# Performance work log

Hardware: AMD Instinct MI355X
Metric: run time of the kernel (lower is better)

## Reference

```python
import jax, jax.numpy as jnp
import numpy as np

GRID_SIZE = 5
SPLINE_ORDER = 3
N_COEFF = GRID_SIZE + SPLINE_ORDER  # 8 basis functions per input feature
D_MODEL = 1024
D_FF = 4096


def make_grid(in_features):
    # uniform grid on [-1, 1] extended by spline_order knots each side
    h = 2.0 / GRID_SIZE
    g = np.arange(-SPLINE_ORDER, GRID_SIZE + SPLINE_ORDER + 1, dtype=np.float32) * h - 1.0
    return jnp.asarray(np.tile(g[None, :], (in_features, 1)))  # (in, G + 2k + 1)


def b_splines(x, grid):
    # x: (N, in) -> (N, in, G + k) via Cox-de Boor recursion
    xe = x[..., None]
    bases = ((xe >= grid[:, :-1]) & (xe < grid[:, 1:])).astype(x.dtype)
    for j in range(1, SPLINE_ORDER + 1):
        left = (xe - grid[:, : -(j + 1)]) / (grid[:, j:-1] - grid[:, : -(j + 1)])
        right = (grid[:, j + 1 :] - xe) / (grid[:, j + 1 :] - grid[:, 1:-j])
        bases = left * bases[..., :-1] + right * bases[..., 1:]
    return bases


def kan_linear(x, base_w, spline_w, grid):
    # x: (N, in); base_w: (out, in); spline_w: (out, in, C)
    base = jax.nn.silu(x) @ base_w.T
    b = b_splines(x, grid)                      # (N, in, C)
    spl = jnp.einsum('nic,oic->no', b, spline_w)
    return base + spl


def setup_inputs() -> dict:
    key = jax.random.key(0)
    ks = jax.random.split(key, 7)
    s_in = 1.0 / np.sqrt(D_MODEL)
    s_ff = 1.0 / np.sqrt(D_FF)
    return {
        'x': jax.random.normal(ks[0], (2, 2048, D_MODEL), jnp.float32),
        'base_w1': jax.random.normal(ks[1], (D_FF, D_MODEL), jnp.float32) * s_in,
        'spline_w1': jax.random.normal(ks[2], (D_FF, D_MODEL, N_COEFF), jnp.float32) * s_in * 0.1,
        'base_w2': jax.random.normal(ks[3], (D_FF, D_MODEL), jnp.float32) * s_in,
        'spline_w2': jax.random.normal(ks[4], (D_FF, D_MODEL, N_COEFF), jnp.float32) * s_in * 0.1,
        'base_w3': jax.random.normal(ks[5], (D_MODEL, D_FF), jnp.float32) * s_ff,
        'spline_w3': jax.random.normal(ks[6], (D_MODEL, D_FF, N_COEFF), jnp.float32) * s_ff * 0.1,
        'grid_in': make_grid(D_MODEL),
        'grid_ff': make_grid(D_FF),
    }


def reference(x, base_w1, spline_w1, base_w2, spline_w2, base_w3, spline_w3, grid_in, grid_ff):
    shp = x.shape
    x2 = x.reshape(-1, shp[-1])                      # (N, d_model)
    h = kan_linear(x2, base_w1, spline_w1, grid_in) * kan_linear(x2, base_w2, spline_w2, grid_in)
    out = kan_linear(h, base_w3, spline_w3, grid_ff)
    return out.reshape(shp)
```

## Files before the change

### kernel.cpp

```cpp
#include <hip/hip_runtime.h>
#include <hip/hip_bf16.h>
#include <cstdint>
#include <cstddef>
#include <type_traits>


#define D_MODEL 1024
#define D_FF    4096
#define NTOK    4096
#define NC      9
#define K1      (D_MODEL * NC)
#define K3      (D_FF * NC)
#define SPLITK2 16
#define SPLITKF 4
#define CHUNK   1024
#define SLOT    65536

typedef __attribute__((ext_vector_type(8))) short bf16x8;
typedef __attribute__((ext_vector_type(4))) float f32x4;

__device__ __forceinline__ unsigned short bf16b(float f) {
  __hip_bfloat16 h = __float2bfloat16(f);
  return __builtin_bit_cast(unsigned short, h);
}

__device__ __forceinline__ void kan_feat_u(float x, unsigned short* dst) {
  float s = x / (1.0f + __expf(-x));
  float B[11];
#pragma unroll
  for (int j = 0; j < 11; ++j) {
    float gj = -2.2f + 0.4f * j;
    B[j] = (x >= gj && x < gj + 0.4f) ? 1.0f : 0.0f;
  }
#pragma unroll
  for (int p = 1; p <= 3; ++p) {
    float inv = 1.0f / (0.4f * p);
#pragma unroll
    for (int i = 0; i + p < 11; ++i) {
      float gi = -2.2f + 0.4f * i;
      B[i] = (x - gi) * inv * B[i] + ((gi + 0.4f + 0.4f * p) - x) * inv * B[i + 1];
    }
  }
  dst[0] = bf16b(s);
#pragma unroll
  for (int c = 0; c < 8; ++c) dst[1 + c] = bf16b(B[c]);
}

__global__ void pack_kan_w(const float* __restrict__ bw, const float* __restrict__ sw,
                           __hip_bfloat16* __restrict__ W, int K, int inShift,
                           int rowMul, int rowBase, size_t totalPairs) {
  size_t t = (size_t)blockIdx.x * blockDim.x + threadIdx.x;
  if (t >= totalPairs) return;
  size_t o = t >> (inShift - 1);
  size_t ip = (t & (((size_t)1 << (inShift - 1)) - 1)) * 2;
  size_t e0 = (o << inShift) + ip;
  float2 b = *(const float2*)(bw + e0);
  const float4* sp = (const float4*)(sw + e0 * 8);
  float4 s0 = sp[0], s1 = sp[1], s2 = sp[2], s3 = sp[3];
  unsigned short h[18];
  h[0] = bf16b(b.x);
  h[1] = bf16b(s0.x); h[2] = bf16b(s0.y); h[3] = bf16b(s0.z); h[4] = bf16b(s0.w);
  h[5] = bf16b(s1.x); h[6] = bf16b(s1.y); h[7] = bf16b(s1.z); h[8] = bf16b(s1.w);
  h[9] = bf16b(b.y);
  h[10] = bf16b(s2.x); h[11] = bf16b(s2.y); h[12] = bf16b(s2.z); h[13] = bf16b(s2.w);
  h[14] = bf16b(s3.x); h[15] = bf16b(s3.y); h[16] = bf16b(s3.z); h[17] = bf16b(s3.w);
  uint32_t* dst = (uint32_t*)(W + (o * rowMul + rowBase) * (size_t)K + ip * NC);
#pragma unroll
  for (int k = 0; k < 9; ++k) dst[k] = (uint32_t)h[2 * k] | ((uint32_t)h[2 * k + 1] << 16);
}

__global__ void build_a1(const float* __restrict__ x, __hip_bfloat16* __restrict__ A1) {
  size_t t = (size_t)blockIdx.x * blockDim.x + threadIdx.x;
  if (t >= (size_t)NTOK * D_MODEL / 2) return;
  size_t n = t >> 9;
  size_t ip = (t & 511) * 2;
  float2 xv = *(const float2*)(x + n * D_MODEL + ip);
  unsigned short h[18];
  kan_feat_u(xv.x, h);
  kan_feat_u(xv.y, h + 9);
  uint32_t* dst = (uint32_t*)(A1 + n * (size_t)K1 + ip * NC);
#pragma unroll
  for (int k = 0; k < 9; ++k) dst[k] = (uint32_t)h[2 * k] | ((uint32_t)h[2 * k + 1] << 16);
}

template <typename HT>
__global__ void glu_a3(const HT* __restrict__ Hc, __hip_bfloat16* __restrict__ A3c) {
  size_t t = (size_t)blockIdx.x * blockDim.x + threadIdx.x;
  if (t >= (size_t)CHUNK * D_FF / 2) return;
  size_t n = t >> 11;
  size_t jp = (t & 2047) * 2;
  float a0, a1, c0, c1;
  if constexpr (std::is_same<HT, float>::value) {
    float2 u = *(const float2*)(Hc + n * 8192 + jp);
    float2 v = *(const float2*)(Hc + n * 8192 + 4096 + jp);
    a0 = u.x; a1 = u.y; c0 = v.x; c1 = v.y;
  } else {
    a0 = __bfloat162float(Hc[n * 8192 + jp]);
    a1 = __bfloat162float(Hc[n * 8192 + jp + 1]);
    c0 = __bfloat162float(Hc[n * 8192 + 4096 + jp]);
    c1 = __bfloat162float(Hc[n * 8192 + 4096 + jp + 1]);
  }
  unsigned short h[18];
  kan_feat_u(a0 * c0, h);
  kan_feat_u(a1 * c1, h + 9);
  uint32_t* dst = (uint32_t*)(A3c + n * (size_t)K3 + jp * NC);
#pragma unroll
  for (int k = 0; k < 9; ++k) dst[k] = (uint32_t)h[2 * k] | ((uint32_t)h[2 * k + 1] << 16);
}

#define STAGE(Ts)                                                                        \
  {                                                                                      \
    const int _sl = ((Ts) & 1) * SLOT;                                                   \
    const size_t _ko = (size_t)(Ts) * 128;                                               \
    _Pragma("unroll") for (int _st = 0; _st < 4; ++_st) {                                \
      __builtin_amdgcn_global_load_lds(                                                  \
          (const __attribute__((address_space(1))) void*)(gA0 + _st * strideK + _ko),    \
          (__attribute__((address_space(3))) void*)(lds_raw + _sl + _st * 8192 + dW),    \
          16, 0, 0);                                                                     \
      __builtin_amdgcn_global_load_lds(                                                  \
          (const __attribute__((address_space(1))) void*)(gB0 + _st * strideK + _ko),    \
          (__attribute__((address_space(3))) void*)(lds_raw + _sl + 32768 +              \
                                                    _st * 8192 + dW),                    \
          16, 0, 0);                                                                     \
    }                                                                                    \
  }

template <typename CT, bool FUSE>
__global__ __launch_bounds__(512, 2) void gemm256(
    const __hip_bfloat16* __restrict__ A, const __hip_bfloat16* __restrict__ Bw,
    CT* __restrict__ Cp, int N, int K, int kLen,
    __hip_bfloat16* __restrict__ A3out) {
  __shared__ __align__(16) char lds_raw[2 * SLOT];

  const int tid = threadIdx.x;
  const int wid = tid >> 6, lane = tid & 63;
  const int wr = wid >> 2, wc = wid & 3;

  const int nwg = gridDim.x * gridDim.y;
  const int orig = blockIdx.y * gridDim.x + blockIdx.x;
  const int q = nwg >> 3, r = nwg & 7;
  const int xcd = orig & 7, lid = orig >> 3;
  const int wg = (xcd < r ? xcd * (q + 1) : r * (q + 1) + (xcd - r) * q) + lid;
  const int bx = wg % gridDim.x, by = wg / gridDim.x;

  const size_t brow = (size_t)by * 256;
  const size_t bcol = (size_t)bx * 256;
  const int kStart = (int)blockIdx.z * kLen;
  const int NT = kLen / 64;

  const int kbx = (lane & 7) ^ (lane >> 3);
  const int rsub = lane >> 3;
  const size_t strideK = (size_t)K * 128;
  const char* gA0 = (const char*)A +
      ((brow + (size_t)(wid * 8 + rsub)) * (size_t)K + kStart + kbx * 8) * 2;
  const char* gB0 = (const char*)Bw +
      ((bcol + (size_t)(wid * 8 + rsub)) * (size_t)K + kStart + kbx * 8) * 2;
  const int dW = wid * 1024;

  const int gx0 = (((lane >> 4) ^ (lane & 7))) * 16;
  const int gx1 = ((((lane >> 4) + 4) ^ (lane & 7))) * 16;
  const int arow = (wr * 128 + (lane & 15)) * 128;
  const int brw = 32768 + (wc * 64 + (lane & 15)) * 128;

  f32x4 acc[8][4] = {};

  STAGE(0);
  asm volatile("s_waitcnt vmcnt(0)" ::: "memory");
  __builtin_amdgcn_s_barrier();

  for (int T = 0; T < NT; ++T) {
    if (T + 1 < NT) STAGE(T + 1);

    const int sl = (T & 1) * SLOT;
    bf16x8 af[8], bfr[4];
#pragma unroll
    for (int mf = 0; mf < 8; ++mf)
      af[mf] = *(const bf16x8*)(lds_raw + sl + arow + mf * 2048 + gx0);
#pragma unroll
    for (int nf = 0; nf < 4; ++nf)
      bfr[nf] = *(const bf16x8*)(lds_raw + sl + brw + nf * 2048 + gx0);
    __builtin_amdgcn_s_setprio(1);
#pragma unroll
    for (int mf = 0; mf < 8; ++mf)
#pragma unroll
      for (int nf = 0; nf < 4; ++nf)
        acc[mf][nf] =
            __builtin_amdgcn_mfma_f32_16x16x32_bf16(af[mf], bfr[nf], acc[mf][nf], 0, 0, 0);
    __builtin_amdgcn_s_setprio(0);
#pragma unroll
    for (int mf = 0; mf < 8; ++mf)
      af[mf] = *(const bf16x8*)(lds_raw + sl + arow + mf * 2048 + gx1);
#pragma unroll
    for (int nf = 0; nf < 4; ++nf)
      bfr[nf] = *(const bf16x8*)(lds_raw + sl + brw + nf * 2048 + gx1);
    __builtin_amdgcn_s_setprio(1);
#pragma unroll
    for (int mf = 0; mf < 8; ++mf)
#pragma unroll
      for (int nf = 0; nf < 4; ++nf)
        acc[mf][nf] =
            __builtin_amdgcn_mfma_f32_16x16x32_bf16(af[mf], bfr[nf], acc[mf][nf], 0, 0, 0);
    __builtin_amdgcn_s_setprio(0);

    asm volatile("s_waitcnt vmcnt(0)" ::: "memory");
    asm volatile("s_waitcnt lgkmcnt(0)" ::: "memory");
    __builtin_amdgcn_s_barrier();
  }

  if constexpr (FUSE) {
    float* gbuf = (float*)lds_raw;
#pragma unroll
    for (int mf = 0; mf < 8; ++mf) {
      const int s = wr * 8 + mf;
#pragma unroll
      for (int nf = 0; nf < 4; ++nf) {
#pragma unroll
        for (int rr = 0; rr < 4; ++rr) {
          float v = acc[mf][nf][rr];
          float w = __shfl_xor(v, 1, 64);
          if (!(lane & 1)) {
            const int r4 = (lane >> 4) * 4 + rr;
            const int ploc = wc * 32 + nf * 8 + ((lane & 14) >> 1);
            gbuf[s * 2048 + r4 * 128 + ploc] = v * w;
          }
        }
      }
    }
    __builtin_amdgcn_s_barrier();
    const int p2 = tid & 63;
    const int rb = tid >> 6;
    for (int k = 0; k < 32; ++k) {
      const int rr_ = rb + 8 * k;
      const int s = rr_ >> 4, rl = rr_ & 15;
      float g0 = gbuf[s * 2048 + rl * 128 + 2 * p2];
      float g1 = gbuf[s * 2048 + rl * 128 + 2 * p2 + 1];
      unsigned short h[18];
      kan_feat_u(g0, h);
      kan_feat_u(g1, h + 9);
      const size_t n = brow + rr_;
      const size_t pg = (bcol >> 1) + 2 * p2;
      uint32_t* dst = (uint32_t*)(A3out + n * (size_t)K3 + pg * NC);
#pragma unroll
      for (int qq = 0; qq < 9; ++qq)
        dst[qq] = (uint32_t)h[2 * qq] | ((uint32_t)h[2 * qq + 1] << 16);
    }
  } else {
#pragma unroll
    for (int mf = 0; mf < 8; ++mf)
#pragma unroll
      for (int nf = 0; nf < 4; ++nf) {
        const size_t r0 = brow + wr * 128 + mf * 16 + (lane >> 4) * 4;
        const size_t c0 = bcol + wc * 64 + nf * 16 + (lane & 15);
        const size_t M = (size_t)gridDim.y * 256;
        CT* C = Cp + (size_t)blockIdx.z * M * (size_t)N;
#pragma unroll
        for (int rr = 0; rr < 4; ++rr) {
          float v = acc[mf][nf][rr];
          if constexpr (std::is_same<CT, float>::value)
            C[(r0 + rr) * (size_t)N + c0] = v;
          else
            C[(r0 + rr) * (size_t)N + c0] = __float2bfloat16(v);
        }
      }
  }
}

__global__ void reduceK(const float* __restrict__ P, float* __restrict__ out,
                        size_t quarter, int nslice) {
  size_t t = (size_t)blockIdx.x * blockDim.x + threadIdx.x;
  if (t >= quarter) return;
  const float4* p = (const float4*)P;
  float4 a = p[t];
  for (int s = 1; s < nslice; ++s) {
    float4 b = p[(size_t)s * quarter + t];
    a.x += b.x; a.y += b.y; a.z += b.z; a.w += b.w;
  }
  ((float4*)out)[t] = a;
}

extern "C" void kernel_launch(void* const* d_in, const int* in_sizes, int n_in,
                              void* d_out, int out_size, void* d_ws, size_t ws_size,
                              hipStream_t stream) {
  const float* x   = (const float*)d_in[0];
  const float* bw1 = (const float*)d_in[1];
  const float* sw1 = (const float*)d_in[2];
  const float* bw2 = (const float*)d_in[3];
  const float* sw2 = (const float*)d_in[4];
  const float* bw3 = (const float*)d_in[5];
  const float* sw3 = (const float*)d_in[6];
  float* out = (float*)d_out;
  char* ws = (char*)d_ws;

  const size_t W12_B  = (size_t)8192 * K1 * 2;
  const size_t A1_B   = (size_t)NTOK * K1 * 2;
  const size_t A3F_B  = (size_t)NTOK * K3 * 2;
  const size_t A3C_B  = (size_t)CHUNK * K3 * 2;
  const size_t HF32_B = (size_t)NTOK * 8192 * 4;

  const bool fused = ws_size >= W12_B + A1_B + A3F_B;
  const bool hF32  = ws_size >= W12_B + A1_B + HF32_B;

  __hip_bfloat16* W12 = (__hip_bfloat16*)(ws);
  __hip_bfloat16* A1  = (__hip_bfloat16*)(ws + W12_B);
  __hip_bfloat16* W3  = A1;

  size_t pairs12 = (size_t)D_FF * D_MODEL / 2;
  int blocks12 = (int)((pairs12 + 255) / 256);
  size_t pairs3 = (size_t)D_MODEL * D_FF / 2;
  int blocks3 = (int)((pairs3 + 255) / 256);
  size_t pairsA1 = (size_t)NTOK * D_MODEL / 2;

  if (fused) {
    __hip_bfloat16* A3f = (__hip_bfloat16*)(ws + W12_B + A1_B);
    float*          Par = (float*)(ws);

    pack_kan_w<<<blocks12, 256, 0, stream>>>(bw1, sw1, W12, K1, 10, 2, 0, pairs12);
    pack_kan_w<<<blocks12, 256, 0, stream>>>(bw2, sw2, W12, K1, 10, 2, 1, pairs12);
    build_a1<<<(int)((pairsA1 + 255) / 256), 256, 0, stream>>>(x, A1);
    gemm256<float, true><<<dim3(8192 / 256, NTOK / 256, 1), 512, 0, stream>>>(
        A1, W12, nullptr, 8192, K1, K1, A3f);
    pack_kan_w<<<blocks3, 256, 0, stream>>>(bw3, sw3, W3, K3, 12, 1, 0, pairs3);
    gemm256<float, false><<<dim3(D_MODEL / 256, NTOK / 256, SPLITKF), 512, 0, stream>>>(
        A3f, W3, Par, D_MODEL, K3, K3 / SPLITKF, nullptr);
    size_t quarter = (size_t)NTOK * D_MODEL / 4;
    reduceK<<<(int)((quarter + 255) / 256), 256, 0, stream>>>(Par, out, quarter, SPLITKF);
  } else {
    void*           Hv  = (void*)(ws + W12_B + A1_B);
    __hip_bfloat16* A3c = (__hip_bfloat16*)(ws);
    float*          Par = (float*)(ws + A3C_B);

    pack_kan_w<<<blocks12, 256, 0, stream>>>(bw1, sw1, W12, K1, 10, 1, 0, pairs12);
    pack_kan_w<<<blocks12, 256, 0, stream>>>(bw2, sw2, W12, K1, 10, 1, 4096, pairs12);
    build_a1<<<(int)((pairsA1 + 255) / 256), 256, 0, stream>>>(x, A1);
    if (hF32)
      gemm256<float, false><<<dim3(8192 / 256, NTOK / 256, 1), 512, 0, stream>>>(
          A1, W12, (float*)Hv, 8192, K1, K1, nullptr);
    else
      gemm256<__hip_bfloat16, false><<<dim3(8192 / 256, NTOK / 256, 1), 512, 0, stream>>>(
          A1, W12, (__hip_bfloat16*)Hv, 8192, K1, K1, nullptr);
    pack_kan_w<<<blocks3, 256, 0, stream>>>(bw3, sw3, W3, K3, 12, 1, 0, pairs3);
    for (int c = 0; c < NTOK / CHUNK; ++c) {
      size_t pairsG = (size_t)CHUNK * D_FF / 2;
      int blocksG = (int)((pairsG + 255) / 256);
      if (hF32)
        glu_a3<float><<<blocksG, 256, 0, stream>>>(
            (const float*)Hv + (size_t)c * CHUNK * 8192, A3c);
      else
        glu_a3<__hip_bfloat16><<<blocksG, 256, 0, stream>>>(
            (const __hip_bfloat16*)Hv + (size_t)c * CHUNK * 8192, A3c);
      gemm256<float, false><<<dim3(D_MODEL / 256, CHUNK / 256, SPLITK2), 512, 0, stream>>>(
          A3c, W3, Par, D_MODEL, K3, K3 / SPLITK2, nullptr);
      size_t quarter = (size_t)CHUNK * D_MODEL / 4;
      reduceK<<<(int)((quarter + 255) / 256), 256, 0, stream>>>(
          Par, out + (size_t)c * CHUNK * D_MODEL, quarter, SPLITK2);
    }
  }
}
```

Measured before the change: 1.040 ms.

## Load GEMM A fragments directly from global memory instead of staging through LDS

Result: slower. 2.349 ms (+125.9%).

```diff
diff --git a/kernel.cpp b/kernel.cpp
--- a/kernel.cpp
+++ b/kernel.cpp
@@ -14,7 +14,7 @@
 #define SPLITK2 16
 #define SPLITKF 4
 #define CHUNK   1024
-#define SLOT    65536
+#define SLOT    32768
 
 typedef __attribute__((ext_vector_type(8))) short bf16x8;
 typedef __attribute__((ext_vector_type(4))) float f32x4;
@@ -108,19 +108,14 @@
   for (int k = 0; k < 9; ++k) dst[k] = (uint32_t)h[2 * k] | ((uint32_t)h[2 * k + 1] << 16);
 }
 
-#define STAGE(Ts)                                                                        \
+#define STAGE_B(Ts)                                                                      \
   {                                                                                      \
     const int _sl = ((Ts) & 1) * SLOT;                                                   \
     const size_t _ko = (size_t)(Ts) * 128;                                               \
     _Pragma("unroll") for (int _st = 0; _st < 4; ++_st) {                                \
       __builtin_amdgcn_global_load_lds(                                                  \
-          (const __attribute__((address_space(1))) void*)(gA0 + _st * strideK + _ko),    \
+          (const __attribute__((address_space(1))) void*)(gB0 + _st * strideK + _ko),    \
           (__attribute__((address_space(3))) void*)(lds_raw + _sl + _st * 8192 + dW),    \
-          16, 0, 0);                                                                     \
-      __builtin_amdgcn_global_load_lds(                                                  \
-          (const __attribute__((address_space(1))) void*)(gB0 + _st * strideK + _ko),    \
-          (__attribute__((address_space(3))) void*)(lds_raw + _sl + 32768 +              \
-                                                    _st * 8192 + dW),                    \
           16, 0, 0);                                                                     \
     }                                                                                    \
   }
@@ -130,7 +125,7 @@
     const __hip_bfloat16* __restrict__ A, const __hip_bfloat16* __restrict__ Bw,
     CT* __restrict__ Cp, int N, int K, int kLen,
     __hip_bfloat16* __restrict__ A3out) {
-  __shared__ __align__(16) char lds_raw[2 * SLOT];
+  __shared__ __align__(16) char lds_raw[131072];
 
   const int tid = threadIdx.x;
   const int wid = tid >> 6, lane = tid & 63;
@@ -151,31 +146,35 @@
   const int kbx = (lane & 7) ^ (lane >> 3);
   const int rsub = lane >> 3;
   const size_t strideK = (size_t)K * 128;
-  const char* gA0 = (const char*)A +
-      ((brow + (size_t)(wid * 8 + rsub)) * (size_t)K + kStart + kbx * 8) * 2;
   const char* gB0 = (const char*)Bw +
       ((bcol + (size_t)(wid * 8 + rsub)) * (size_t)K + kStart + kbx * 8) * 2;
   const int dW = wid * 1024;
 
   const int gx0 = (((lane >> 4) ^ (lane & 7))) * 16;
   const int gx1 = ((((lane >> 4) + 4) ^ (lane & 7))) * 16;
-  const int arow = (wr * 128 + (lane & 15)) * 128;
-  const int brw = 32768 + (wc * 64 + (lane & 15)) * 128;
+  const int brw = (wc * 64 + (lane & 15)) * 128;
+
+  const __hip_bfloat16* aBase =
+      A + (brow + (size_t)(wr * 128 + (lane & 15))) * (size_t)K + kStart + (lane >> 4) * 8;
 
   f32x4 acc[8][4] = {};
 
-  STAGE(0);
+  STAGE_B(0);
   asm volatile("s_waitcnt vmcnt(0)" ::: "memory");
   __builtin_amdgcn_s_barrier();
 
   for (int T = 0; T < NT; ++T) {
-    if (T + 1 < NT) STAGE(T + 1);
+    if (T + 1 < NT) STAGE_B(T + 1);
 
     const int sl = (T & 1) * SLOT;
-    bf16x8 af[8], bfr[4];
-#pragma unroll
-    for (int mf = 0; mf < 8; ++mf)
-      af[mf] = *(const bf16x8*)(lds_raw + sl + arow + mf * 2048 + gx0);
+    const __hip_bfloat16* aT = aBase + (size_t)T * 64;
+    bf16x8 af0[8], af1[8], bfr[4];
+#pragma unroll
+    for (int mf = 0; mf < 8; ++mf)
+      af0[mf] = *(const bf16x8*)(aT + (size_t)mf * 16 * K);
+#pragma unroll
+    for (int mf = 0; mf < 8; ++mf)
+      af1[mf] = *(const bf16x8*)(aT + (size_t)mf * 16 * K + 32);
 #pragma unroll
     for (int nf = 0; nf < 4; ++nf)
       bfr[nf] = *(const bf16x8*)(lds_raw + sl + brw + nf * 2048 + gx0);
@@ -185,11 +184,8 @@
 #pragma unroll
       for (int nf = 0; nf < 4; ++nf)
         acc[mf][nf] =
-            __builtin_amdgcn_mfma_f32_16x16x32_bf16(af[mf], bfr[nf], acc[mf][nf], 0, 0, 0);
+            __builtin_amdgcn_mfma_f32_16x16x32_bf16(af0[mf], bfr[nf], acc[mf][nf], 0, 0, 0);
     __builtin_amdgcn_s_setprio(0);
-#pragma unroll
-    for (int mf = 0; mf < 8; ++mf)
-      af[mf] = *(const bf16x8*)(lds_raw + sl + arow + mf * 2048 + gx1);
 #pragma unroll
     for (int nf = 0; nf < 4; ++nf)
       bfr[nf] = *(const bf16x8*)(lds_raw + sl + brw + nf * 2048 + gx1);
@@ -199,7 +195,7 @@
 #pragma unroll
       for (int nf = 0; nf < 4; ++nf)
         acc[mf][nf] =
-            __builtin_amdgcn_mfma_f32_16x16x32_bf16(af[mf], bfr[nf], acc[mf][nf], 0, 0, 0);
+            __builtin_amdgcn_mfma_f32_16x16x32_bf16(af1[mf], bfr[nf], acc[mf][nf], 0, 0, 0);
     __builtin_amdgcn_s_setprio(0);
 
     asm volatile("s_waitcnt vmcnt(0)" ::: "memory");
```

## Switch KAN feature/weight packing to feature-major pair layout for coalesced stores

Applied to the files above, without the earlier changes.

New measurement: 1.012 ms. 2.6% less time.

```diff
diff --git a/kernel.cpp b/kernel.cpp
--- a/kernel.cpp
+++ b/kernel.cpp
@@ -23,6 +23,9 @@
   __hip_bfloat16 h = __float2bfloat16(f);
   return __builtin_bit_cast(unsigned short, h);
 }
+__device__ __forceinline__ uint32_t pk2(float a, float b) {
+  return (uint32_t)bf16b(a) | ((uint32_t)bf16b(b) << 16);
+}
 
 __device__ __forceinline__ void kan_feat_u(float x, unsigned short* dst) {
   float s = x / (1.0f + __expf(-x));
@@ -51,36 +54,39 @@
                            int rowMul, int rowBase, size_t totalPairs) {
   size_t t = (size_t)blockIdx.x * blockDim.x + threadIdx.x;
   if (t >= totalPairs) return;
-  size_t o = t >> (inShift - 1);
-  size_t ip = (t & (((size_t)1 << (inShift - 1)) - 1)) * 2;
-  size_t e0 = (o << inShift) + ip;
+  const int halfShift = inShift - 1;
+  size_t o = t >> halfShift;
+  size_t p = t & (((size_t)1 << halfShift) - 1);
+  size_t e0 = (o << inShift) + 2 * p;
   float2 b = *(const float2*)(bw + e0);
   const float4* sp = (const float4*)(sw + e0 * 8);
   float4 s0 = sp[0], s1 = sp[1], s2 = sp[2], s3 = sp[3];
-  unsigned short h[18];
-  h[0] = bf16b(b.x);
-  h[1] = bf16b(s0.x); h[2] = bf16b(s0.y); h[3] = bf16b(s0.z); h[4] = bf16b(s0.w);
-  h[5] = bf16b(s1.x); h[6] = bf16b(s1.y); h[7] = bf16b(s1.z); h[8] = bf16b(s1.w);
-  h[9] = bf16b(b.y);
-  h[10] = bf16b(s2.x); h[11] = bf16b(s2.y); h[12] = bf16b(s2.z); h[13] = bf16b(s2.w);
-  h[14] = bf16b(s3.x); h[15] = bf16b(s3.y); h[16] = bf16b(s3.z); h[17] = bf16b(s3.w);
-  uint32_t* dst = (uint32_t*)(W + (o * rowMul + rowBase) * (size_t)K + ip * NC);
-#pragma unroll
-  for (int k = 0; k < 9; ++k) dst[k] = (uint32_t)h[2 * k] | ((uint32_t)h[2 * k + 1] << 16);
+  const size_t HP = (size_t)1 << halfShift;
+  uint32_t* dst = (uint32_t*)(W + (o * rowMul + rowBase) * (size_t)K);
+  dst[p]          = pk2(b.x, b.y);
+  dst[1 * HP + p] = pk2(s0.x, s2.x);
+  dst[2 * HP + p] = pk2(s0.y, s2.y);
+  dst[3 * HP + p] = pk2(s0.z, s2.z);
+  dst[4 * HP + p] = pk2(s0.w, s2.w);
+  dst[5 * HP + p] = pk2(s1.x, s3.x);
+  dst[6 * HP + p] = pk2(s1.y, s3.y);
+  dst[7 * HP + p] = pk2(s1.z, s3.z);
+  dst[8 * HP + p] = pk2(s1.w, s3.w);
 }
 
 __global__ void build_a1(const float* __restrict__ x, __hip_bfloat16* __restrict__ A1) {
   size_t t = (size_t)blockIdx.x * blockDim.x + threadIdx.x;
   if (t >= (size_t)NTOK * D_MODEL / 2) return;
   size_t n = t >> 9;
-  size_t ip = (t & 511) * 2;
-  float2 xv = *(const float2*)(x + n * D_MODEL + ip);
-  unsigned short h[18];
-  kan_feat_u(xv.x, h);
-  kan_feat_u(xv.y, h + 9);
-  uint32_t* dst = (uint32_t*)(A1 + n * (size_t)K1 + ip * NC);
-#pragma unroll
-  for (int k = 0; k < 9; ++k) dst[k] = (uint32_t)h[2 * k] | ((uint32_t)h[2 * k + 1] << 16);
+  size_t p = t & 511;
+  float2 xv = *(const float2*)(x + n * D_MODEL + 2 * p);
+  unsigned short h0[9], h1[9];
+  kan_feat_u(xv.x, h0);
+  kan_feat_u(xv.y, h1);
+  uint32_t* dst = (uint32_t*)(A1 + n * (size_t)K1);
+#pragma unroll
+  for (int f = 0; f < 9; ++f)
+    dst[(size_t)f * 512 + p] = (uint32_t)h0[f] | ((uint32_t)h1[f] << 16);
 }
 
 template <typename HT>
@@ -88,24 +94,25 @@
   size_t t = (size_t)blockIdx.x * blockDim.x + threadIdx.x;
   if (t >= (size_t)CHUNK * D_FF / 2) return;
   size_t n = t >> 11;
-  size_t jp = (t & 2047) * 2;
+  size_t p = t & 2047;
   float a0, a1, c0, c1;
   if constexpr (std::is_same<HT, float>::value) {
-    float2 u = *(const float2*)(Hc + n * 8192 + jp);
-    float2 v = *(const float2*)(Hc + n * 8192 + 4096 + jp);
+    float2 u = *(const float2*)(Hc + n * 8192 + 2 * p);
+    float2 v = *(const float2*)(Hc + n * 8192 + 4096 + 2 * p);
     a0 = u.x; a1 = u.y; c0 = v.x; c1 = v.y;
   } else {
-    a0 = __bfloat162float(Hc[n * 8192 + jp]);
-    a1 = __bfloat162float(Hc[n * 8192 + jp + 1]);
-    c0 = __bfloat162float(Hc[n * 8192 + 4096 + jp]);
-    c1 = __bfloat162float(Hc[n * 8192 + 4096 + jp + 1]);
-  }
-  unsigned short h[18];
-  kan_feat_u(a0 * c0, h);
-  kan_feat_u(a1 * c1, h + 9);
-  uint32_t* dst = (uint32_t*)(A3c + n * (size_t)K3 + jp * NC);
-#pragma unroll
-  for (int k = 0; k < 9; ++k) dst[k] = (uint32_t)h[2 * k] | ((uint32_t)h[2 * k + 1] << 16);
+    a0 = __bfloat162float(Hc[n * 8192 + 2 * p]);
+    a1 = __bfloat162float(Hc[n * 8192 + 2 * p + 1]);
+    c0 = __bfloat162float(Hc[n * 8192 + 4096 + 2 * p]);
+    c1 = __bfloat162float(Hc[n * 8192 + 4096 + 2 * p + 1]);
+  }
+  unsigned short h0[9], h1[9];
+  kan_feat_u(a0 * c0, h0);
+  kan_feat_u(a1 * c1, h1);
+  uint32_t* dst = (uint32_t*)(A3c + n * (size_t)K3);
+#pragma unroll
+  for (int f = 0; f < 9; ++f)
+    dst[(size_t)f * 2048 + p] = (uint32_t)h0[f] | ((uint32_t)h1[f] << 16);
 }
 
 #define STAGE(Ts)                                                                        \
@@ -234,15 +241,14 @@
       const int s = rr_ >> 4, rl = rr_ & 15;
       float g0 = gbuf[s * 2048 + rl * 128 + 2 * p2];
       float g1 = gbuf[s * 2048 + rl * 128 + 2 * p2 + 1];
-      unsigned short h[18];
-      kan_feat_u(g0, h);
-      kan_feat_u(g1, h + 9);
-      const size_t n = brow + rr_;
-      const size_t pg = (bcol >> 1) + 2 * p2;
-      uint32_t* dst = (uint32_t*)(A3out + n * (size_t)K3 + pg * NC);
-#pragma unroll
-      for (int qq = 0; qq < 9; ++qq)
-        dst[qq] = (uint32_t)h[2 * qq] | ((uint32_t)h[2 * qq + 1] << 16);
+      unsigned short h0[9], h1[9];
+      kan_feat_u(g0, h0);
+      kan_feat_u(g1, h1);
+      uint32_t* dst = (uint32_t*)(A3out + (brow + rr_) * (size_t)K3);
+      const size_t pbase = (bcol >> 2) + p2;
+#pragma unroll
+      for (int f = 0; f < 9; ++f)
+        dst[(size_t)f * 2048 + pbase] = (uint32_t)h0[f] | ((uint32_t)h1[f] << 16);
     }
   } else {
 #pragma unroll
```
